# Kernel tuning notes

Measured on AMD Instinct MI355X. Metric: run time of the kernel, lower is better.

Reference implementation:

```python
import jax, jax.numpy as jnp
import numpy as np

MOE_TOPK = 2


def setup_inputs() -> dict:
    key = jax.random.key(0)
    k1, k2 = jax.random.split(key, 2)
    hidden_states = jax.random.normal(k1, (4, 4096, 2048), dtype=jnp.float32)
    gate_w = jax.random.normal(k2, (2048, 64), dtype=jnp.float32) * 0.02
    gate_b = jnp.zeros((64,), dtype=jnp.float32)
    return {"hidden_states": hidden_states, "gate_w": gate_w, "gate_b": gate_b}


def reference(hidden_states, gate_w, gate_b):
    # flatten [B, S, D] -> [N, D]
    x = hidden_states.reshape(-1, hidden_states.shape[-1])
    # gate linear: [N, E]
    logits = jnp.einsum("nd,de->ne", x, gate_w) + gate_b
    # stable softmax; torch detaches the max (no grad through max path)
    logits_max = jax.lax.stop_gradient(jnp.max(logits, axis=-1, keepdims=True))
    probs = jax.nn.softmax(logits - logits_max, axis=-1)
    # top-k selection + renormalize
    topk_vals, topk_idx = jax.lax.top_k(probs, MOE_TOPK)
    if MOE_TOPK == 1:
        norm_vals = jnp.ones_like(topk_vals)
    else:
        sum_vals = jnp.clip(jnp.sum(topk_vals, axis=-1, keepdims=True), 1e-6, None)
        norm_vals = topk_vals / sum_vals
    return logits, norm_vals, topk_idx
```

## Files before the change

kernel.cpp:

```cpp
#include <hip/hip_runtime.h>
#include <hip/hip_bf16.h>

#define NTOK 16384
#define DIM  2048
#define NE   64
#define TPB  64
#define NTILE 2
#define KG   8
#define KPW  (DIM / KG)
#define KSTEPS (KPW / 32)
#define NKS_ALL (DIM / 32)
#define LP   65

typedef __attribute__((ext_vector_type(8))) short  short8;
typedef __attribute__((ext_vector_type(4))) float  f32x4;

static __device__ __forceinline__ unsigned short f2bf(float f) {
    unsigned u = __float_as_uint(f);
    unsigned r = (u + 0x7fffu + ((u >> 16) & 1u)) >> 16;
    return (unsigned short)r;
}
static __device__ __forceinline__ float bf2f(unsigned short h) {
    return __uint_as_float(((unsigned)h) << 16);
}

static __device__ __forceinline__ void cvt_pair(float x0, float x1,
                                                unsigned& hi, unsigned& lo) {
    union { __hip_bfloat162 b; unsigned u; } h, l;
    h.b = __float22bfloat162_rn(float2{x0, x1});
    float h0 = __uint_as_float(h.u << 16);
    float h1 = __uint_as_float(h.u & 0xffff0000u);
    l.b = __float22bfloat162_rn(float2{x0 - h0, x1 - h1});
    hi = h.u; lo = l.u;
}

__global__ void pack_w(const float* __restrict__ W,
                       unsigned short* __restrict__ WH,
                       unsigned short* __restrict__ WL) {
    int idx = blockIdx.x * 256 + threadIdx.x;
    if (idx >= DIM * NE) return;
    int k = idx / NE, e = idx % NE;
    float w = W[idx];
    unsigned short h = f2bf(w);
    unsigned short l = f2bf(w - bf2f(h));
    int etile = e >> 4, col = e & 15;
    int kstep = k >> 5, lsub = (k >> 3) & 3, j = k & 7;
    size_t off = (((size_t)etile * NKS_ALL + kstep) * 64 + (lsub * 16 + col)) * 8 + j;
    WH[off] = h;
    WL[off] = l;
}

__global__ __launch_bounds__(1024, 4) void router_mfma(
    const float* __restrict__ X,
    const unsigned short* __restrict__ WH,
    const unsigned short* __restrict__ WL,
    const float* __restrict__ B, float* __restrict__ out)
{
    __shared__ float red[KG][TPB][LP];
    __shared__ float lg[TPB][LP];

    const int tid  = threadIdx.x;
    const int lane = tid & 63;
    const int wv   = tid >> 6;
    const int kg   = __builtin_amdgcn_readfirstlane(wv & 7);
    const int th   = __builtin_amdgcn_readfirstlane(wv >> 3);
    const int t0   = blockIdx.x * TPB;

    const int arow = lane & 15;
    const int koff = (lane >> 4) * 8;

    const float* xp0 = X + (size_t)(t0 + th * 32 + arow) * DIM + kg * KPW + koff;
    const float* xp1 = xp0 + (size_t)16 * DIM;

    f32x4 acc[NTILE][4];
#pragma unroll
    for (int t = 0; t < NTILE; ++t)
#pragma unroll
        for (int et = 0; et < 4; ++et) acc[t][et] = (f32x4){0.f, 0.f, 0.f, 0.f};

#pragma unroll 2
    for (int s = 0; s < KSTEPS; ++s) {
        float4 xa0 = *(const float4*)(xp0 + s * 32);
        float4 xb0 = *(const float4*)(xp0 + s * 32 + 4);
        float4 xa1 = *(const float4*)(xp1 + s * 32);
        float4 xb1 = *(const float4*)(xp1 + s * 32 + 4);

        const int ks = kg * KSTEPS + s;
        short8 bh[4], bl[4];
#pragma unroll
        for (int et = 0; et < 4; ++et) {
            size_t foff = (((size_t)et * NKS_ALL + ks) * 64 + lane) * 8;
            bh[et] = *(const short8*)(WH + foff);
            bl[et] = *(const short8*)(WL + foff);
        }

        union { unsigned u[4]; short8 s8; } ah[NTILE], al[NTILE];
        cvt_pair(xa0.x, xa0.y, ah[0].u[0], al[0].u[0]);
        cvt_pair(xa0.z, xa0.w, ah[0].u[1], al[0].u[1]);
        cvt_pair(xb0.x, xb0.y, ah[0].u[2], al[0].u[2]);
        cvt_pair(xb0.z, xb0.w, ah[0].u[3], al[0].u[3]);
        cvt_pair(xa1.x, xa1.y, ah[1].u[0], al[1].u[0]);
        cvt_pair(xa1.z, xa1.w, ah[1].u[1], al[1].u[1]);
        cvt_pair(xb1.x, xb1.y, ah[1].u[2], al[1].u[2]);
        cvt_pair(xb1.z, xb1.w, ah[1].u[3], al[1].u[3]);

#pragma unroll
        for (int et = 0; et < 4; ++et) {
#pragma unroll
            for (int t = 0; t < NTILE; ++t) {
                acc[t][et] = __builtin_amdgcn_mfma_f32_16x16x32_bf16(ah[t].s8, bh[et], acc[t][et], 0, 0, 0);
                acc[t][et] = __builtin_amdgcn_mfma_f32_16x16x32_bf16(ah[t].s8, bl[et], acc[t][et], 0, 0, 0);
                acc[t][et] = __builtin_amdgcn_mfma_f32_16x16x32_bf16(al[t].s8, bh[et], acc[t][et], 0, 0, 0);
            }
        }
    }

#pragma unroll
    for (int t = 0; t < NTILE; ++t)
#pragma unroll
        for (int et = 0; et < 4; ++et)
#pragma unroll
            for (int r = 0; r < 4; ++r)
                red[kg][th * 32 + t * 16 + (lane >> 4) * 4 + r][et * 16 + (lane & 15)] = acc[t][et][r];
    __syncthreads();

    float* out_nv  = out + (size_t)NTOK * NE;
    float* out_idx = out_nv + (size_t)NTOK * 2;

    {
        const int rt = tid >> 4;
        const int re = (tid & 15) * 4;
        float4 s = {0.f, 0.f, 0.f, 0.f};
#pragma unroll
        for (int g = 0; g < KG; ++g) {
            s.x += red[g][rt][re + 0];
            s.y += red[g][rt][re + 1];
            s.z += red[g][rt][re + 2];
            s.w += red[g][rt][re + 3];
        }
        float4 bb = *(const float4*)(B + re);
        s.x += bb.x; s.y += bb.y; s.z += bb.z; s.w += bb.w;
        *(float4*)&out[(size_t)(t0 + rt) * NE + re] = s;
        lg[rt][re + 0] = s.x;
        lg[rt][re + 1] = s.y;
        lg[rt][re + 2] = s.z;
        lg[rt][re + 3] = s.w;
    }
    __syncthreads();

    if (tid < 4 * TPB) {
        const int tt = tid >> 2;
        const int q  = tid & 3;
        float m1 = -1e30f, m2 = -1e30f;
        int   i1 = 0, i2 = 0;
#pragma unroll
        for (int j = 0; j < 16; ++j) {
            int   e = q * 16 + j;
            float v = lg[tt][e];
            if (v > m1)      { m2 = m1; i2 = i1; m1 = v; i1 = e; }
            else if (v > m2) { m2 = v;  i2 = e; }
        }
#pragma unroll
        for (int d = 1; d <= 2; d <<= 1) {
            float om1 = __shfl_xor(m1, d);
            int   oi1 = __shfl_xor(i1, d);
            float om2 = __shfl_xor(m2, d);
            int   oi2 = __shfl_xor(i2, d);
            bool agt = (m1 > om1) || (m1 == om1 && i1 < oi1);
            float a1 = agt ? m1 : om1;  int ai1 = agt ? i1 : oi1;
            float c2 = agt ? m2 : om2;  int ci2 = agt ? i2 : oi2;
            float c1 = agt ? om1 : m1;  int ci1 = agt ? oi1 : i1;
            bool sgt = (c2 > c1) || (c2 == c1 && ci2 < ci1);
            m1 = a1; i1 = ai1;
            m2 = sgt ? c2 : c1; i2 = sgt ? ci2 : ci1;
        }
        if (q == 0) {
            float e2  = expf(m2 - m1);
            float inv = 1.f / (1.f + e2);
            int t = t0 + tt;
            out_nv[t * 2 + 0]  = inv;
            out_nv[t * 2 + 1]  = e2 * inv;
            out_idx[t * 2 + 0] = (float)i1;
            out_idx[t * 2 + 1] = (float)i2;
        }
    }
}

extern "C" void kernel_launch(void* const* d_in, const int* in_sizes, int n_in,
                              void* d_out, int out_size, void* d_ws, size_t ws_size,
                              hipStream_t stream) {
    const float* X = (const float*)d_in[0];
    const float* W = (const float*)d_in[1];
    const float* B = (const float*)d_in[2];
    float* out = (float*)d_out;

    unsigned short* WH = (unsigned short*)d_ws;
    unsigned short* WL = WH + (size_t)DIM * NE;

    hipLaunchKernelGGL(pack_w, dim3((DIM * NE + 255) / 256), dim3(256), 0, stream, W, WH, WL);
    hipLaunchKernelGGL(router_mfma, dim3(NTOK / TPB), dim3(1024), 0, stream, X, WH, WL, B, out);
}
```

Measured before the change: 38.79 us.

## Give each wave four token tiles with double-buffered register prefetch

Each block now runs 8 waves of 512 threads instead of 16, and each wave covers all 64 tokens of its K-group as four MFMA row tiles. That halves the weight-fragment loads per block and reuses each B fragment across more tokens. The K loop is unrolled into an explicit two-stage register double buffer, so X and W loads for the next step are issued before the current step's MFMAs. The separate logits LDS buffer is dropped and red[0] is reused, which lowers shared memory use. In exchange, accumulator and buffer register pressure rises and there are fewer waves per block to hide memory latency.

Measured after the change: 36.71 us. 1.06x faster.

```diff
diff --git a/kernel.cpp b/kernel.cpp
--- a/kernel.cpp
+++ b/kernel.cpp
@@ -5,7 +5,7 @@
 #define DIM  2048
 #define NE   64
 #define TPB  64
-#define NTILE 2
+#define NTILE 4
 #define KG   8
 #define KPW  (DIM / KG)
 #define KSTEPS (KPW / 32)
@@ -50,27 +50,28 @@
     WL[off] = l;
 }
 
-__global__ __launch_bounds__(1024, 4) void router_mfma(
+__global__ __launch_bounds__(512, 2) void router_mfma(
     const float* __restrict__ X,
     const unsigned short* __restrict__ WH,
     const unsigned short* __restrict__ WL,
     const float* __restrict__ B, float* __restrict__ out)
 {
     __shared__ float red[KG][TPB][LP];
-    __shared__ float lg[TPB][LP];
 
     const int tid  = threadIdx.x;
     const int lane = tid & 63;
-    const int wv   = tid >> 6;
-    const int kg   = __builtin_amdgcn_readfirstlane(wv & 7);
-    const int th   = __builtin_amdgcn_readfirstlane(wv >> 3);
+    const int kg   = __builtin_amdgcn_readfirstlane(tid >> 6);
     const int t0   = blockIdx.x * TPB;
 
     const int arow = lane & 15;
     const int koff = (lane >> 4) * 8;
 
-    const float* xp0 = X + (size_t)(t0 + th * 32 + arow) * DIM + kg * KPW + koff;
-    const float* xp1 = xp0 + (size_t)16 * DIM;
+    const float* xp0 = X + (size_t)(t0 +  0 + arow) * DIM + kg * KPW + koff;
+    const float* xp1 = X + (size_t)(t0 + 16 + arow) * DIM + kg * KPW + koff;
+    const float* xp2 = X + (size_t)(t0 + 32 + arow) * DIM + kg * KPW + koff;
+    const float* xp3 = X + (size_t)(t0 + 48 + arow) * DIM + kg * KPW + koff;
+
+    const int ksbase = kg * KSTEPS;
 
     f32x4 acc[NTILE][4];
 #pragma unroll
@@ -78,41 +79,56 @@
 #pragma unroll
         for (int et = 0; et < 4; ++et) acc[t][et] = (f32x4){0.f, 0.f, 0.f, 0.f};
 
-#pragma unroll 2
-    for (int s = 0; s < KSTEPS; ++s) {
-        float4 xa0 = *(const float4*)(xp0 + s * 32);
-        float4 xb0 = *(const float4*)(xp0 + s * 32 + 4);
-        float4 xa1 = *(const float4*)(xp1 + s * 32);
-        float4 xb1 = *(const float4*)(xp1 + s * 32 + 4);
-
-        const int ks = kg * KSTEPS + s;
-        short8 bh[4], bl[4];
-#pragma unroll
-        for (int et = 0; et < 4; ++et) {
-            size_t foff = (((size_t)et * NKS_ALL + ks) * 64 + lane) * 8;
-            bh[et] = *(const short8*)(WH + foff);
-            bl[et] = *(const short8*)(WL + foff);
-        }
-
-        union { unsigned u[4]; short8 s8; } ah[NTILE], al[NTILE];
-        cvt_pair(xa0.x, xa0.y, ah[0].u[0], al[0].u[0]);
-        cvt_pair(xa0.z, xa0.w, ah[0].u[1], al[0].u[1]);
-        cvt_pair(xb0.x, xb0.y, ah[0].u[2], al[0].u[2]);
-        cvt_pair(xb0.z, xb0.w, ah[0].u[3], al[0].u[3]);
-        cvt_pair(xa1.x, xa1.y, ah[1].u[0], al[1].u[0]);
-        cvt_pair(xa1.z, xa1.w, ah[1].u[1], al[1].u[1]);
-        cvt_pair(xb1.x, xb1.y, ah[1].u[2], al[1].u[2]);
-        cvt_pair(xb1.z, xb1.w, ah[1].u[3], al[1].u[3]);
-
-#pragma unroll
-        for (int et = 0; et < 4; ++et) {
-#pragma unroll
-            for (int t = 0; t < NTILE; ++t) {
-                acc[t][et] = __builtin_amdgcn_mfma_f32_16x16x32_bf16(ah[t].s8, bh[et], acc[t][et], 0, 0, 0);
-                acc[t][et] = __builtin_amdgcn_mfma_f32_16x16x32_bf16(ah[t].s8, bl[et], acc[t][et], 0, 0, 0);
-                acc[t][et] = __builtin_amdgcn_mfma_f32_16x16x32_bf16(al[t].s8, bh[et], acc[t][et], 0, 0, 0);
-            }
-        }
+    float4 xA[NTILE][2], xB[NTILE][2];
+    short8 bhA[4], blA[4], bhB[4], blB[4];
+
+#define LOADX(buf, s) do {                                                    \
+    buf[0][0] = *(const float4*)(xp0 + (s) * 32);                             \
+    buf[0][1] = *(const float4*)(xp0 + (s) * 32 + 4);                         \
+    buf[1][0] = *(const float4*)(xp1 + (s) * 32);                             \
+    buf[1][1] = *(const float4*)(xp1 + (s) * 32 + 4);                         \
+    buf[2][0] = *(const float4*)(xp2 + (s) * 32);                             \
+    buf[2][1] = *(const float4*)(xp2 + (s) * 32 + 4);                         \
+    buf[3][0] = *(const float4*)(xp3 + (s) * 32);                             \
+    buf[3][1] = *(const float4*)(xp3 + (s) * 32 + 4);                         \
+  } while (0)
+
+#define LOADB(bh_, bl_, s) do {                                               \
+    _Pragma("unroll")                                                         \
+    for (int et = 0; et < 4; ++et) {                                          \
+        size_t foff = (((size_t)et * NKS_ALL + ksbase + (s)) * 64 + lane) * 8;\
+        bh_[et] = *(const short8*)(WH + foff);                                \
+        bl_[et] = *(const short8*)(WL + foff);                                \
+    }                                                                         \
+  } while (0)
+
+#define COMPUTE(xv, bh_, bl_) do {                                            \
+    union { unsigned u[4]; short8 s8; } ah[NTILE], al[NTILE];                 \
+    _Pragma("unroll")                                                         \
+    for (int t = 0; t < NTILE; ++t) {                                         \
+        cvt_pair(xv[t][0].x, xv[t][0].y, ah[t].u[0], al[t].u[0]);             \
+        cvt_pair(xv[t][0].z, xv[t][0].w, ah[t].u[1], al[t].u[1]);             \
+        cvt_pair(xv[t][1].x, xv[t][1].y, ah[t].u[2], al[t].u[2]);             \
+        cvt_pair(xv[t][1].z, xv[t][1].w, ah[t].u[3], al[t].u[3]);             \
+    }                                                                         \
+    _Pragma("unroll")                                                         \
+    for (int et = 0; et < 4; ++et) {                                          \
+        _Pragma("unroll")                                                     \
+        for (int t = 0; t < NTILE; ++t) {                                     \
+            acc[t][et] = __builtin_amdgcn_mfma_f32_16x16x32_bf16(ah[t].s8, bh_[et], acc[t][et], 0, 0, 0); \
+            acc[t][et] = __builtin_amdgcn_mfma_f32_16x16x32_bf16(ah[t].s8, bl_[et], acc[t][et], 0, 0, 0); \
+            acc[t][et] = __builtin_amdgcn_mfma_f32_16x16x32_bf16(al[t].s8, bh_[et], acc[t][et], 0, 0, 0); \
+        }                                                                     \
+    }                                                                         \
+  } while (0)
+
+    LOADX(xA, 0); LOADB(bhA, blA, 0);
+#pragma unroll
+    for (int ii = 0; ii < KSTEPS / 2; ++ii) {
+        LOADX(xB, 2 * ii + 1); LOADB(bhB, blB, 2 * ii + 1);
+        COMPUTE(xA, bhA, blA);
+        if (ii < KSTEPS / 2 - 1) { LOADX(xA, 2 * ii + 2); LOADB(bhA, blA, 2 * ii + 2); }
+        COMPUTE(xB, bhB, blB);
     }
 
 #pragma unroll
@@ -121,15 +137,17 @@
         for (int et = 0; et < 4; ++et)
 #pragma unroll
             for (int r = 0; r < 4; ++r)
-                red[kg][th * 32 + t * 16 + (lane >> 4) * 4 + r][et * 16 + (lane & 15)] = acc[t][et][r];
+                red[kg][t * 16 + (lane >> 4) * 4 + r][et * 16 + (lane & 15)] = acc[t][et][r];
     __syncthreads();
 
     float* out_nv  = out + (size_t)NTOK * NE;
     float* out_idx = out_nv + (size_t)NTOK * 2;
 
-    {
-        const int rt = tid >> 4;
-        const int re = (tid & 15) * 4;
+#pragma unroll
+    for (int k = 0; k < 2; ++k) {
+        const int idx = tid + k * 512;
+        const int rt = idx >> 4;
+        const int re = (idx & 15) * 4;
         float4 s = {0.f, 0.f, 0.f, 0.f};
 #pragma unroll
         for (int g = 0; g < KG; ++g) {
@@ -141,10 +159,10 @@
         float4 bb = *(const float4*)(B + re);
         s.x += bb.x; s.y += bb.y; s.z += bb.z; s.w += bb.w;
         *(float4*)&out[(size_t)(t0 + rt) * NE + re] = s;
-        lg[rt][re + 0] = s.x;
-        lg[rt][re + 1] = s.y;
-        lg[rt][re + 2] = s.z;
-        lg[rt][re + 3] = s.w;
+        red[0][rt][re + 0] = s.x;
+        red[0][rt][re + 1] = s.y;
+        red[0][rt][re + 2] = s.z;
+        red[0][rt][re + 3] = s.w;
     }
     __syncthreads();
 
@@ -156,7 +174,7 @@
 #pragma unroll
         for (int j = 0; j < 16; ++j) {
             int   e = q * 16 + j;
-            float v = lg[tt][e];
+            float v = red[0][tt][e];
             if (v > m1)      { m2 = m1; i2 = i1; m1 = v; i1 = e; }
             else if (v > m2) { m2 = v;  i2 = e; }
         }
@@ -198,5 +216,5 @@
     unsigned short* WL = WH + (size_t)DIM * NE;
 
     hipLaunchKernelGGL(pack_w, dim3((DIM * NE + 255) / 256), dim3(256), 0, stream, W, WH, WL);
-    hipLaunchKernelGGL(router_mfma, dim3(NTOK / TPB), dim3(1024), 0, stream, X, WH, WL, B, out);
-}
+    hipLaunchKernelGGL(router_mfma, dim3(NTOK / TPB), dim3(512), 0, stream, X, WH, WL, B, out);
+}
```

## Stage X and W chunks through LDS ring with async global_load_lds pipeline

Applied to the files above, without the earlier changes.

Replaces the split-K scheme (8 K-groups whose partial sums are reduced through shared memory) with a full-K loop per wave. X and packed bf16 weights are streamed into a 4-slot LDS ring using direct global-to-LDS loads, with three chunks in flight and explicit vmcnt waits plus barriers. X rows are XOR-swizzled in LDS to avoid bank conflicts, and waves split into 4 token tiles by 2 expert halves. This removes the cross-wave reduction and overlaps memory with MFMA, but drops to 512 threads with 128KB+ LDS, so only one block fits per CU and occupancy is lower.

After: 49.64 us. +28.0%, slower.

```diff
diff --git a/kernel.cpp b/kernel.cpp
--- a/kernel.cpp
+++ b/kernel.cpp
@@ -5,12 +5,10 @@
 #define DIM  2048
 #define NE   64
 #define TPB  64
-#define NTILE 2
-#define KG   8
-#define KPW  (DIM / KG)
-#define KSTEPS (KPW / 32)
+#define NCH  32
+#define RING 4
+#define SLOTB 32768
 #define NKS_ALL (DIM / 32)
-#define LP   65
 
 typedef __attribute__((ext_vector_type(8))) short  short8;
 typedef __attribute__((ext_vector_type(4))) float  f32x4;
@@ -23,7 +21,6 @@
 static __device__ __forceinline__ float bf2f(unsigned short h) {
     return __uint_as_float(((unsigned)h) << 16);
 }
-
 static __device__ __forceinline__ void cvt_pair(float x0, float x1,
                                                 unsigned& hi, unsigned& lo) {
     union { __hip_bfloat162 b; unsigned u; } h, l;
@@ -33,6 +30,11 @@
     l.b = __float22bfloat162_rn(float2{x0 - h0, x1 - h1});
     hi = h.u; lo = l.u;
 }
+
+#define GLOAD_LDS(gp, lp) \
+    __builtin_amdgcn_global_load_lds( \
+        (const __attribute__((address_space(1))) unsigned int*)(const void*)(gp), \
+        (__attribute__((address_space(3))) unsigned int*)(void*)(lp), 16, 0, 0)
 
 __global__ void pack_w(const float* __restrict__ W,
                        unsigned short* __restrict__ WH,
@@ -50,113 +52,137 @@
     WL[off] = l;
 }
 
-__global__ __launch_bounds__(1024, 4) void router_mfma(
+__global__ __launch_bounds__(512, 1) void router_mfma(
     const float* __restrict__ X,
     const unsigned short* __restrict__ WH,
     const unsigned short* __restrict__ WL,
     const float* __restrict__ B, float* __restrict__ out)
 {
-    __shared__ float red[KG][TPB][LP];
-    __shared__ float lg[TPB][LP];
+    __shared__ __align__(16) unsigned char ring[RING * SLOTB];
+    __shared__ float lg[TPB][65];
 
     const int tid  = threadIdx.x;
     const int lane = tid & 63;
     const int wv   = tid >> 6;
-    const int kg   = __builtin_amdgcn_readfirstlane(wv & 7);
-    const int th   = __builtin_amdgcn_readfirstlane(wv >> 3);
+    const int tt   = __builtin_amdgcn_readfirstlane(wv & 3);
+    const int eh   = __builtin_amdgcn_readfirstlane(wv >> 2);
     const int t0   = blockIdx.x * TPB;
 
-    const int arow = lane & 15;
-    const int koff = (lane >> 4) * 8;
-
-    const float* xp0 = X + (size_t)(t0 + th * 32 + arow) * DIM + kg * KPW + koff;
-    const float* xp1 = xp0 + (size_t)16 * DIM;
-
-    f32x4 acc[NTILE][4];
-#pragma unroll
-    for (int t = 0; t < NTILE; ++t)
-#pragma unroll
-        for (int et = 0; et < 4; ++et) acc[t][et] = (f32x4){0.f, 0.f, 0.f, 0.f};
-
-#pragma unroll 2
-    for (int s = 0; s < KSTEPS; ++s) {
-        float4 xa0 = *(const float4*)(xp0 + s * 32);
-        float4 xb0 = *(const float4*)(xp0 + s * 32 + 4);
-        float4 xa1 = *(const float4*)(xp1 + s * 32);
-        float4 xb1 = *(const float4*)(xp1 + s * 32 + 4);
-
-        const int ks = kg * KSTEPS + s;
-        short8 bh[4], bl[4];
-#pragma unroll
-        for (int et = 0; et < 4; ++et) {
-            size_t foff = (((size_t)et * NKS_ALL + ks) * 64 + lane) * 8;
-            bh[et] = *(const short8*)(WH + foff);
-            bl[et] = *(const short8*)(WL + foff);
-        }
-
-        union { unsigned u[4]; short8 s8; } ah[NTILE], al[NTILE];
-        cvt_pair(xa0.x, xa0.y, ah[0].u[0], al[0].u[0]);
-        cvt_pair(xa0.z, xa0.w, ah[0].u[1], al[0].u[1]);
-        cvt_pair(xb0.x, xb0.y, ah[0].u[2], al[0].u[2]);
-        cvt_pair(xb0.z, xb0.w, ah[0].u[3], al[0].u[3]);
-        cvt_pair(xa1.x, xa1.y, ah[1].u[0], al[1].u[0]);
-        cvt_pair(xa1.z, xa1.w, ah[1].u[1], al[1].u[1]);
-        cvt_pair(xb1.x, xb1.y, ah[1].u[2], al[1].u[2]);
-        cvt_pair(xb1.z, xb1.w, ah[1].u[3], al[1].u[3]);
-
-#pragma unroll
-        for (int et = 0; et < 4; ++et) {
-#pragma unroll
-            for (int t = 0; t < NTILE; ++t) {
-                acc[t][et] = __builtin_amdgcn_mfma_f32_16x16x32_bf16(ah[t].s8, bh[et], acc[t][et], 0, 0, 0);
-                acc[t][et] = __builtin_amdgcn_mfma_f32_16x16x32_bf16(ah[t].s8, bl[et], acc[t][et], 0, 0, 0);
-                acc[t][et] = __builtin_amdgcn_mfma_f32_16x16x32_bf16(al[t].s8, bh[et], acc[t][et], 0, 0, 0);
+#define STAGE_CHUNK(c) do {                                                      \
+    unsigned char* slot_ = ring + ((c) & 3) * SLOTB;                             \
+    _Pragma("unroll")                                                            \
+    for (int i_ = 0; i_ < 2; ++i_) {                                             \
+        int row_ = wv * 8 + i_ * 4 + (lane >> 4);                                \
+        int p_   = lane & 15;                                                    \
+        int b_   = (p_ & 8) | ((p_ & 7) ^ (row_ & 7));                           \
+        const float* g_ = X + (size_t)(t0 + row_) * DIM + (c) * 64 + b_ * 4;     \
+        GLOAD_LDS(g_, slot_ + (wv * 2 + i_) * 1024);                             \
+    }                                                                            \
+    _Pragma("unroll")                                                            \
+    for (int i_ = 0; i_ < 2; ++i_) {                                             \
+        int idx_ = wv * 2 + i_;                        \
+        int ksl_ = idx_ >> 3, etg_ = (idx_ >> 1) & 3, hl_ = idx_ & 1;            \
+        int ks_  = (c) * 2 + ksl_;                                               \
+        const unsigned short* s_ = (hl_ ? WL : WH) +                             \
+            (((size_t)etg_ * NKS_ALL + ks_) * 64 + lane) * 8;                    \
+        GLOAD_LDS(s_, slot_ + 16384 + idx_ * 1024);                              \
+    }                                                                            \
+  } while (0)
+
+    f32x4 acc[2];
+    acc[0] = (f32x4){0.f, 0.f, 0.f, 0.f};
+    acc[1] = (f32x4){0.f, 0.f, 0.f, 0.f};
+
+    STAGE_CHUNK(0);
+    STAGE_CHUNK(1);
+    STAGE_CHUNK(2);
+
+    const int g   = lane >> 4;
+    const int r   = lane & 15;
+    const int row = tt * 16 + r;
+
+#pragma unroll 1
+    for (int c = 0; c < NCH; ++c) {
+        if (c < NCH - 2)       asm volatile("s_waitcnt vmcnt(8)" ::: "memory");
+        else if (c == NCH - 2) asm volatile("s_waitcnt vmcnt(4)" ::: "memory");
+        else                   asm volatile("s_waitcnt vmcnt(0)" ::: "memory");
+        __builtin_amdgcn_s_barrier();
+        __builtin_amdgcn_sched_barrier(0);
+
+        if (c + 3 < NCH) STAGE_CHUNK(c + 3);
+        __builtin_amdgcn_sched_barrier(0);
+
+        unsigned char* slot = ring + (c & 3) * SLOTB;
+        const unsigned char* bbase = slot + 16384;
+
+        short8 bh[2][2], bl[2][2];
+#pragma unroll
+        for (int ksl = 0; ksl < 2; ++ksl)
+#pragma unroll
+            for (int et = 0; et < 2; ++et) {
+                int etg = eh * 2 + et;
+                bh[ksl][et] = *(const short8*)(bbase + (ksl * 8 + etg * 2 + 0) * 1024 + lane * 16);
+                bl[ksl][et] = *(const short8*)(bbase + (ksl * 8 + etg * 2 + 1) * 1024 + lane * 16);
             }
-        }
-    }
-
-#pragma unroll
-    for (int t = 0; t < NTILE; ++t)
-#pragma unroll
-        for (int et = 0; et < 4; ++et)
-#pragma unroll
-            for (int r = 0; r < 4; ++r)
-                red[kg][th * 32 + t * 16 + (lane >> 4) * 4 + r][et * 16 + (lane & 15)] = acc[t][et][r];
+
+#pragma unroll
+        for (int cs = 0; cs < 2; ++cs) {
+            int b0 = cs * 8 + 2 * g;
+            int p0 = (b0 & 8) | ((b0 & 7) ^ (r & 7));
+            int p1 = ((b0 + 1) & 8) | (((b0 + 1) & 7) ^ (r & 7));
+            float4 xa = *(const float4*)(slot + row * 256 + p0 * 16);
+            float4 xb = *(const float4*)(slot + row * 256 + p1 * 16);
+
+            union { unsigned u[4]; short8 s8; } ah, al;
+            cvt_pair(xa.x, xa.y, ah.u[0], al.u[0]);
+            cvt_pair(xa.z, xa.w, ah.u[1], al.u[1]);
+            cvt_pair(xb.x, xb.y, ah.u[2], al.u[2]);
+            cvt_pair(xb.z, xb.w, ah.u[3], al.u[3]);
+
+#pragma unroll
+            for (int et = 0; et < 2; ++et) {
+                acc[et] = __builtin_amdgcn_mfma_f32_16x16x32_bf16(ah.s8, bh[cs][et], acc[et], 0, 0, 0);
+                acc[et] = __builtin_amdgcn_mfma_f32_16x16x32_bf16(ah.s8, bl[cs][et], acc[et], 0, 0, 0);
+                acc[et] = __builtin_amdgcn_mfma_f32_16x16x32_bf16(al.s8, bh[cs][et], acc[et], 0, 0, 0);
+            }
+        }
+    }
+
+#pragma unroll
+    for (int et = 0; et < 2; ++et) {
+        int etg = eh * 2 + et;
+        float bias = B[etg * 16 + r];
+#pragma unroll
+        for (int q = 0; q < 4; ++q)
+            lg[tt * 16 + g * 4 + q][etg * 16 + r] = acc[et][q] + bias;
+    }
     __syncthreads();
 
     float* out_nv  = out + (size_t)NTOK * NE;
     float* out_idx = out_nv + (size_t)NTOK * 2;
 
-    {
-        const int rt = tid >> 4;
-        const int re = (tid & 15) * 4;
-        float4 s = {0.f, 0.f, 0.f, 0.f};
-#pragma unroll
-        for (int g = 0; g < KG; ++g) {
-            s.x += red[g][rt][re + 0];
-            s.y += red[g][rt][re + 1];
-            s.z += red[g][rt][re + 2];
-            s.w += red[g][rt][re + 3];
-        }
-        float4 bb = *(const float4*)(B + re);
-        s.x += bb.x; s.y += bb.y; s.z += bb.z; s.w += bb.w;
+#pragma unroll
+    for (int k = 0; k < 2; ++k) {
+        const int idx = tid + k * 512;
+        const int rt = idx >> 4;
+        const int re = (idx & 15) * 4;
+        float4 s;
+        s.x = lg[rt][re + 0];
+        s.y = lg[rt][re + 1];
+        s.z = lg[rt][re + 2];
+        s.w = lg[rt][re + 3];
         *(float4*)&out[(size_t)(t0 + rt) * NE + re] = s;
-        lg[rt][re + 0] = s.x;
-        lg[rt][re + 1] = s.y;
-        lg[rt][re + 2] = s.z;
-        lg[rt][re + 3] = s.w;
-    }
-    __syncthreads();
+    }
 
     if (tid < 4 * TPB) {
-        const int tt = tid >> 2;
+        const int tk = tid >> 2;
         const int q  = tid & 3;
         float m1 = -1e30f, m2 = -1e30f;
         int   i1 = 0, i2 = 0;
 #pragma unroll
         for (int j = 0; j < 16; ++j) {
             int   e = q * 16 + j;
-            float v = lg[tt][e];
+            float v = lg[tk][e];
             if (v > m1)      { m2 = m1; i2 = i1; m1 = v; i1 = e; }
             else if (v > m2) { m2 = v;  i2 = e; }
         }
@@ -177,7 +203,7 @@
         if (q == 0) {
             float e2  = expf(m2 - m1);
             float inv = 1.f / (1.f + e2);
-            int t = t0 + tt;
+            int t = t0 + tk;
             out_nv[t * 2 + 0]  = inv;
             out_nv[t * 2 + 1]  = e2 * inv;
             out_idx[t * 2 + 0] = (float)i1;
@@ -198,5 +224,5 @@
     unsigned short* WL = WH + (size_t)DIM * NE;
 
     hipLaunchKernelGGL(pack_w, dim3((DIM * NE + 255) / 256), dim3(256), 0, stream, W, WH, WL);
-    hipLaunchKernelGGL(router_mfma, dim3(NTOK / TPB), dim3(1024), 0, stream, X, WH, WL, B, out);
-}
+    hipLaunchKernelGGL(router_mfma, dim3(NTOK / TPB), dim3(512), 0, stream, X, WH, WL, B, out);
+}
```
